# Performance work log

Measured on AMD Instinct MI355X. Metric: run time of the kernel, lower is better.

## Reference

```python
import jax, jax.numpy as jnp
import numpy as np

SEQ_LEN = 4096
EMBED_DIM = 1280
NUM_HEADS = 16
HEAD_DIM = EMBED_DIM // NUM_HEADS  # 80
SCALING = float(np.sqrt(HEAD_DIM))  # NOTE: source multiplies by sqrt(head_dim)
NEG_INF = float(np.finfo(np.float32).min)


def rotate_half(x):
    x1, x2 = jnp.split(x, 2, axis=-1)
    return jnp.concatenate((-x2, x1), axis=-1)


def setup_inputs() -> dict:
    key = jax.random.key(0)
    ks = jax.random.split(key, 7)
    s = 0.02
    hidden_states = jax.random.normal(ks[0], (SEQ_LEN, EMBED_DIM), dtype=jnp.float32)
    w_qkv = jax.random.normal(ks[1], (3 * EMBED_DIM, EMBED_DIM), dtype=jnp.float32) * s
    b_qkv = jax.random.normal(ks[2], (3 * EMBED_DIM,), dtype=jnp.float32) * s
    w_proj = jax.random.normal(ks[3], (EMBED_DIM, EMBED_DIM), dtype=jnp.float32) * s
    b_proj = jax.random.normal(ks[4], (EMBED_DIM,), dtype=jnp.float32) * s
    # rotary angles: theta duplicated to head_dim (emb = cat(rope, rope))
    inv_freq = 1.0 / (10000.0 ** (jnp.arange(0, HEAD_DIM // 2, dtype=jnp.float32) * 2.0 / HEAD_DIM))
    pos = jnp.arange(SEQ_LEN, dtype=jnp.float32)
    freqs = pos[:, None] * inv_freq[None, :]            # [S, hd/2]
    emb = jnp.concatenate((freqs, freqs), axis=-1)       # [S, hd]
    cos = jnp.cos(emb)
    sin = jnp.sin(emb)
    # 4 packed images of 1024 patches each
    cu_seqlens = jnp.array([0, 1024, 2048, 3072, 4096], dtype=jnp.int32)
    return {
        "hidden_states": hidden_states,
        "w_qkv": w_qkv, "b_qkv": b_qkv,
        "w_proj": w_proj, "b_proj": b_proj,
        "cos": cos, "sin": sin,
        "cu_seqlens": cu_seqlens,
    }


def reference(hidden_states, w_qkv, b_qkv, w_proj, b_proj, cos, sin, cu_seqlens):
    S = hidden_states.shape[0]
    # packed QKV projection
    qkv = hidden_states @ w_qkv.T + b_qkv                  # [S, 3D]
    qkv = qkv.reshape(S, 3, NUM_HEADS, HEAD_DIM)
    q, k, v = qkv[:, 0], qkv[:, 1], qkv[:, 2]              # [S, H, hd]
    # fp32 RoPE (broadcast cos/sin over heads)
    c = cos[:, None, :].astype(jnp.float32)
    sn = sin[:, None, :].astype(jnp.float32)
    qf, kf = q.astype(jnp.float32), k.astype(jnp.float32)
    q = (qf * c + rotate_half(qf) * sn).astype(q.dtype)
    k = (kf * c + rotate_half(kf) * sn).astype(k.dtype)
    # block-diagonal mask from cu_seqlens: same segment -> 0, else -inf
    pos = jnp.arange(S)
    seg = jnp.searchsorted(cu_seqlens, pos, side="right") - 1  # [S]
    bias = jnp.where(seg[:, None] == seg[None, :], 0.0, NEG_INF)  # [S, S]
    # dense attention over whole packed sequence (as in source)
    scores = jnp.einsum("shd,thd->hst", q, k) * SCALING + bias[None]
    weights = jax.nn.softmax(scores.astype(jnp.float32), axis=-1).astype(q.dtype)
    attn = jnp.einsum("hst,thd->shd", weights, v).reshape(S, EMBED_DIM)
    return attn @ w_proj.T + b_proj
```

## Files before the change

### kernel.cpp

```cpp
#include <hip/hip_runtime.h>

#define SEQ   4096
#define EMB   1280
#define NH    16
#define HD    80
#define HDP   96
#define O3    3840
#define SEGLEN 1024
#define NSEG  4
#define QSCALE (8.94427190999915878564f * 1.44269504088896340736f)

typedef unsigned short u16;
typedef __attribute__((ext_vector_type(8))) _Float16 f16x8;
typedef __attribute__((ext_vector_type(4))) _Float16 f16x4;
typedef __attribute__((ext_vector_type(2))) __fp16   h16x2;
typedef __attribute__((ext_vector_type(4))) float    f32x4;

__device__ __forceinline__ float ex2(float x) { return __builtin_amdgcn_exp2f(x); }

__device__ __forceinline__ u16 f2h(float f) {
  union { _Float16 h; u16 u; } v; v.h = (_Float16)f; return v.u;
}
__device__ __forceinline__ float h2f(u16 b) {
  union { u16 u; _Float16 h; } v; v.u = b; return (float)v.h;
}
__device__ __forceinline__ f32x4 exp2_4(f32x4 x) {
  f32x4 r; r.x = ex2(x.x); r.y = ex2(x.y); r.z = ex2(x.z); r.w = ex2(x.w); return r;
}
__device__ __forceinline__ f16x4 pk4(f32x4 s) {
  union { h16x2 h[2]; f16x4 f; } u;
  u.h[0] = __builtin_amdgcn_cvt_pkrtz(s.x, s.y);
  u.h[1] = __builtin_amdgcn_cvt_pkrtz(s.z, s.w);
  return u.f;
}
__device__ __forceinline__ void gl2lds16(const u16* g, u16* l) {
  __builtin_amdgcn_global_load_lds(
      (const __attribute__((address_space(1))) unsigned int*)g,
      (__attribute__((address_space(3))) unsigned int*)l, 16, 0, 0);
}

#define CVT_N1 (SEQ * EMB / 4)
#define CVT_N2 (O3 * EMB / 4)
#define CVT_N3 (EMB * EMB / 4)
__global__ void cvt_all_kernel(const float* __restrict__ a, const float* __restrict__ b,
                               const float* __restrict__ c, u16* __restrict__ oa,
                               u16* __restrict__ ob, u16* __restrict__ oc) {
  int i = blockIdx.x * blockDim.x + threadIdx.x;
  const float* src; u16* dst; int j = i;
  if (j < CVT_N1)                { src = a; dst = oa; }
  else if (j < CVT_N1 + CVT_N2)  { src = b; dst = ob; j -= CVT_N1; }
  else                           { src = c; dst = oc; j -= CVT_N1 + CVT_N2; }
  float4 f = ((const float4*)src)[j];
  union { u16 h[4]; uint2 v; } o;
  o.h[0] = f2h(f.x); o.h[1] = f2h(f.y); o.h[2] = f2h(f.z); o.h[3] = f2h(f.w);
  ((uint2*)dst)[j] = o.v;
}

template<int OUTF>
__global__ __launch_bounds__(256)
void gemm_bias_kernel(const u16* __restrict__ A, const u16* __restrict__ W,
                      const float* __restrict__ bias, void* __restrict__ Cout,
                      int N, int K) {
  __shared__ u16 As[128][64];
  __shared__ u16 Bs[128][64];
  const int tid  = threadIdx.x;
  const int bm   = blockIdx.y, bn = blockIdx.x;
  const int lane = tid & 63;
  const int wid  = tid >> 6;
  const int wm   = (wid >> 1) * 64, wn = (wid & 1) * 64;
  const int lr   = lane & 15, quad = lane >> 4;

  f32x4 acc[4][4];
  const f32x4 z4 = {0.f, 0.f, 0.f, 0.f};
  #pragma unroll
  for (int i = 0; i < 4; ++i)
    #pragma unroll
    for (int j = 0; j < 4; ++j) acc[i][j] = z4;

  const int arow = tid >> 3;
  const int acol = (((tid & 7) ^ (arow & 7)) * 8);
  const u16* Ab = A + (size_t)(bm * 128) * K;
  const u16* Wb = W + (size_t)(bn * 128) * K;
  u16* AsL = &As[0][0] + tid * 8;
  u16* BsL = &Bs[0][0] + tid * 8;

  for (int kt = 0; kt < K; kt += 64) {
    #pragma unroll
    for (int r = 0; r < 4; ++r) {
      gl2lds16(&Ab[(size_t)(arow + r * 32) * K + kt + acol], AsL + r * 2048);
      gl2lds16(&Wb[(size_t)(arow + r * 32) * K + kt + acol], BsL + r * 2048);
    }
    __syncthreads();
    #pragma unroll
    for (int k32 = 0; k32 < 2; ++k32) {
      const int c = (((k32 * 4 + quad) ^ (lr & 7)) * 8);
      f16x8 aF[4], bF[4];
      #pragma unroll
      for (int i = 0; i < 4; ++i) {
        aF[i] = *(const f16x8*)&As[wm + i * 16 + lr][c];
        bF[i] = *(const f16x8*)&Bs[wn + i * 16 + lr][c];
      }
      #pragma unroll
      for (int i = 0; i < 4; ++i)
        #pragma unroll
        for (int j = 0; j < 4; ++j)
          acc[i][j] = __builtin_amdgcn_mfma_f32_16x16x32_f16(aF[i], bF[j], acc[i][j], 0, 0, 0);
    }
    __syncthreads();
  }

  #pragma unroll
  for (int i = 0; i < 4; ++i) {
    int rowb = bm * 128 + wm + i * 16 + quad * 4;
    #pragma unroll
    for (int j = 0; j < 4; ++j) {
      int col = bn * 128 + wn + j * 16 + lr;
      float bv = bias[col];
      #pragma unroll
      for (int r = 0; r < 4; ++r) {
        float v = acc[i][j][r] + bv;
        if (OUTF) ((float*)Cout)[(size_t)(rowb + r) * N + col] = v;
        else      ((u16*)Cout)[(size_t)(rowb + r) * N + col] = f2h(v);
      }
    }
  }
}

__global__ __launch_bounds__(512, 2)
void gemm256_kernel(const u16* __restrict__ A, const u16* __restrict__ W,
                    const float* __restrict__ bias, u16* __restrict__ Cout,
                    int N, int K) {
  __shared__ u16 As[2][256][64];
  __shared__ u16 Bs[2][256][64];
  const int tid  = threadIdx.x;
  const int bm   = blockIdx.y, bn = blockIdx.x;
  const int lane = tid & 63;
  const int wid  = tid >> 6;
  const int wm   = wid >> 2;
  const int wn   = wid & 3;
  const int lr   = lane & 15, quad = lane >> 4;
  const int NT   = K >> 6;

  const u16* Ab = A + (size_t)(bm * 256) * K;
  const u16* Wb = W + (size_t)(bn * 256) * K;

  const int srr  = tid >> 3;
  const int scol = ((tid & 7) ^ (srr & 7)) << 3;
  const u16* ApL = Ab + (size_t)srr * K + scol;
  const u16* WpL = Wb + (size_t)srr * K + scol;

  auto stA = [&](int b, int row0, int t) {
    gl2lds16(ApL + (size_t)row0 * K + t * 64,        &As[b][row0][0]      + tid * 8);
    gl2lds16(ApL + (size_t)(row0 + 64) * K + t * 64, &As[b][row0 + 64][0] + tid * 8);
  };
  auto stB = [&](int b, int row0, int t) {
    gl2lds16(WpL + (size_t)row0 * K + t * 64,        &Bs[b][row0][0]      + tid * 8);
    gl2lds16(WpL + (size_t)(row0 + 64) * K + t * 64, &Bs[b][row0 + 64][0] + tid * 8);
  };

  f32x4 acc[8][4];
  const f32x4 z4 = {0.f, 0.f, 0.f, 0.f};
  #pragma unroll
  for (int i = 0; i < 8; ++i)
    #pragma unroll
    for (int j = 0; j < 4; ++j) acc[i][j] = z4;

  stA(0, 0, 0); stA(0, 128, 0);
  stB(0, 0, 0); stB(0, 128, 0);
  stA(1, 0, 1);
  asm volatile("s_waitcnt vmcnt(2)" ::: "memory");
  __builtin_amdgcn_s_barrier();

  for (int t = 0; t < NT; ++t) {
    const int buf = t & 1, nb = buf ^ 1;
    #pragma unroll
    for (int mq = 0; mq < 2; ++mq) {
      #pragma unroll
      for (int k32 = 0; k32 < 2; ++k32) {
        const int c = (((k32 * 4 + quad) ^ (lr & 7)) << 3);
        f16x8 aF[4], bF[4];
        #pragma unroll
        for (int i = 0; i < 4; ++i)
          aF[i] = *(const f16x8*)&As[buf][mq * 128 + wm * 64 + i * 16 + lr][c];
        #pragma unroll
        for (int j = 0; j < 4; ++j)
          bF[j] = *(const f16x8*)&Bs[buf][wn * 64 + j * 16 + lr][c];
        __builtin_amdgcn_sched_barrier(0);
        if (mq == 0 && k32 == 0) {
          if (t + 1 < NT) { stB(nb, 0, t + 1); stA(nb, 128, t + 1); }
        } else if (mq == 0 && k32 == 1) {
          if (t + 1 < NT) stB(nb, 128, t + 1);
        } else if (mq == 1 && k32 == 0) {
          if (t + 2 < NT) stA(buf, 0, t + 2);
        }
        __builtin_amdgcn_s_barrier();
        asm volatile("s_waitcnt lgkmcnt(0)" ::: "memory");
        __builtin_amdgcn_sched_barrier(0);
        __builtin_amdgcn_s_setprio(1);
        #pragma unroll
        for (int i = 0; i < 4; ++i)
          #pragma unroll
          for (int j = 0; j < 4; ++j)
            acc[mq * 4 + i][j] =
                __builtin_amdgcn_mfma_f32_16x16x32_f16(aF[i], bF[j], acc[mq * 4 + i][j], 0, 0, 0);
        __builtin_amdgcn_s_setprio(0);
        if (mq == 1 && k32 == 1) {
          if (t < NT - 2) asm volatile("s_waitcnt vmcnt(2)" ::: "memory");
          else            asm volatile("s_waitcnt vmcnt(0)" ::: "memory");
        }
        __builtin_amdgcn_s_barrier();
        __builtin_amdgcn_sched_barrier(0);
      }
    }
  }

  #pragma unroll
  for (int mq = 0; mq < 2; ++mq) {
    #pragma unroll
    for (int i = 0; i < 4; ++i) {
      const int rowb = bm * 256 + mq * 128 + wm * 64 + i * 16 + quad * 4;
      #pragma unroll
      for (int j = 0; j < 4; ++j) {
        const int col = bn * 256 + wn * 64 + j * 16 + lr;
        const float bv = bias[col];
        #pragma unroll
        for (int r = 0; r < 4; ++r)
          Cout[(size_t)(rowb + r) * N + col] = f2h(acc[mq * 4 + i][j][r] + bv);
      }
    }
  }
}

__global__ __launch_bounds__(256)
void rope_reorg_kernel(const u16* __restrict__ qkv, const float* __restrict__ cosp,
                       const float* __restrict__ sinp, u16* __restrict__ Qp,
                       u16* __restrict__ Kp, u16* __restrict__ Vt) {
  __shared__ u16 Qs[64][80];
  __shared__ u16 Ks[64][80];
  __shared__ u16 Vs[64][88];
  const int tid = threadIdx.x;
  const int s0 = blockIdx.x * 64;
  const int h  = blockIdx.y;

  for (int t = tid; t < 640; t += 256) {
    int r = t / 10, c = (t % 10) * 8;
    size_t g = (size_t)(s0 + r) * O3 + h * HD + c;
    *(uint4*)&Qs[r][c] = *(const uint4*)&qkv[g];
    *(uint4*)&Ks[r][c] = *(const uint4*)&qkv[g + EMB];
    *(uint4*)&Vs[r][c] = *(const uint4*)&qkv[g + 2 * EMB];
  }
  __syncthreads();

  for (int t = tid; t < 64 * 24; t += 256) {
    int r = t / 24, d4 = (t % 24) * 4;
    int s = s0 + r;
    size_t po = ((size_t)h * SEQ + s) * HDP + d4;
    if (d4 >= HD) {
      uint2 z = make_uint2(0, 0);
      *(uint2*)&Qp[po] = z; *(uint2*)&Kp[po] = z;
      continue;
    }
    float4 cv = *(const float4*)&cosp[(size_t)s * HD + d4];
    float4 sv = *(const float4*)&sinp[(size_t)s * HD + d4];
    int dp4 = (d4 < 40) ? d4 + 40 : d4 - 40;
    float sgn = (d4 < 40) ? -1.f : 1.f;
    union { u16 h[4]; uint2 v; } oq, ok;
    const float* cp = (const float*)&cv;
    const float* sp = (const float*)&sv;
    #pragma unroll
    for (int j = 0; j < 4; ++j) {
      float q  = h2f(Qs[r][d4 + j]),  k  = h2f(Ks[r][d4 + j]);
      float qp = h2f(Qs[r][dp4 + j]), kp = h2f(Ks[r][dp4 + j]);
      oq.h[j] = f2h((q * cp[j] + sgn * qp * sp[j]) * QSCALE);
      ok.h[j] = f2h(k * cp[j] + sgn * kp * sp[j]);
    }
    *(uint2*)&Qp[po] = oq.v;
    *(uint2*)&Kp[po] = ok.v;
  }

  for (int t = tid; t < HD * 8; t += 256) {
    int d = t / 8, sc = (t % 8) * 8;
    union { u16 h[8]; uint4 v; } o;
    #pragma unroll
    for (int j = 0; j < 8; ++j) o.h[j] = Vs[sc + j][d];
    *(uint4*)&Vt[((size_t)(h * HD + d)) * SEQ + s0 + sc] = o.v;
  }
}

__global__ __launch_bounds__(256)
void attn_kernel(const u16* __restrict__ Qp, const u16* __restrict__ Kp,
                 const u16* __restrict__ Vt, u16* __restrict__ attnO) {
  __shared__ u16 K_l[64][96];
  __shared__ u16 V_l[96][64];

  const int tid = threadIdx.x;
  const int lane = tid & 63, w = tid >> 6;
  const int lr = lane & 15, quad = lane >> 4;
  const int h = blockIdx.y, sg = blockIdx.z;
  const int seg0 = sg * SEGLEN;
  const int q0b = seg0 + blockIdx.x * 64;

  f16x8 qF[3];
  {
    int qrow = q0b + w * 16 + lr;
    #pragma unroll
    for (int kc = 0; kc < 3; ++kc)
      qF[kc] = *(const f16x8*)&Qp[((size_t)h * SEQ + qrow) * HDP + kc * 32 + quad * 8];
  }

  {
    u16 val = (tid < 16) ? (u16)0x3C00 : (u16)0;
    u16* q = &V_l[80][0] + tid * 4;
    q[0] = val; q[1] = val; q[2] = val; q[3] = val;
  }

  const u16* Kbase = Kp + ((size_t)h * SEQ + seg0) * HDP;
  const u16* Vbase = Vt + (size_t)h * HD * SEQ + seg0;
  const u16* pK[3]; u16* dK[3];
  const u16* pV[3]; u16* dV[3];
  #pragma unroll
  for (int t = 0; t < 3; ++t) {
    int s = t * 256 + tid;
    int r = s / 12, c = s % 12;
    int ck = (c & ~3) | ((c & 3) ^ ((r >> 1) & 3));
    pK[t] = Kbase + (size_t)r * HDP + ck * 8;
    dK[t] = &K_l[0][0] + s * 8;
    int rv = s / 8, cv = s % 8;
    int cg = cv ^ (rv & 7);
    pV[t] = Vbase + (size_t)rv * SEQ + cg * 8;
    dV[t] = &V_l[0][0] + s * 8;
  }

  const f32x4 z4 = {0.f, 0.f, 0.f, 0.f};
  float m_r = -3.0e38f;
  f32x4 Oacc[6];
  #pragma unroll
  for (int n = 0; n < 6; ++n) Oacc[n] = z4;

  const int kswz = (lr >> 1) & 3;

  for (int kt = 0; kt < SEGLEN; kt += 64) {
    gl2lds16(pK[0], dK[0]); gl2lds16(pK[1], dK[1]); gl2lds16(pK[2], dK[2]);
    gl2lds16(pV[0], dV[0]); gl2lds16(pV[1], dV[1]);
    if (tid < 128) gl2lds16(pV[2], dV[2]);
    #pragma unroll
    for (int t = 0; t < 3; ++t) { pK[t] += 64 * HDP; pV[t] += 64; }
    __syncthreads();

    f32x4 S[4];
    __builtin_amdgcn_s_setprio(1);
    #pragma unroll
    for (int ct = 0; ct < 4; ++ct) {
      S[ct] = z4;
      #pragma unroll
      for (int kc = 0; kc < 3; ++kc) {
        f16x8 kF = *(const f16x8*)&K_l[ct * 16 + lr][kc * 32 + ((quad ^ kswz) << 3)];
        S[ct] = __builtin_amdgcn_mfma_f32_16x16x32_f16(kF, qF[kc], S[ct], 0, 0, 0);
      }
    }
    __builtin_amdgcn_s_setprio(0);

    float mx = fmaxf(fmaxf(S[0].x, S[0].y), fmaxf(S[0].z, S[0].w));
    #pragma unroll
    for (int ct = 1; ct < 4; ++ct)
      mx = fmaxf(mx, fmaxf(fmaxf(S[ct].x, S[ct].y), fmaxf(S[ct].z, S[ct].w)));
    mx = fmaxf(mx, __shfl_xor(mx, 16, 64));
    mx = fmaxf(mx, __shfl_xor(mx, 32, 64));
    float mnew = fmaxf(m_r, mx);
    float alpha = ex2(m_r - mnew);
    m_r = mnew;

    f32x4 mv = {mnew, mnew, mnew, mnew};
    #pragma unroll
    for (int ct = 0; ct < 4; ++ct) S[ct] = exp2_4(S[ct] - mv);

    if (__ballot(alpha != 1.0f)) {
      f32x4 al;
      al.x = __shfl(alpha, quad * 4 + 0, 64);
      al.y = __shfl(alpha, quad * 4 + 1, 64);
      al.z = __shfl(alpha, quad * 4 + 2, 64);
      al.w = __shfl(alpha, quad * 4 + 3, 64);
      #pragma unroll
      for (int n = 0; n < 6; ++n) Oacc[n] *= al;
    }

    f16x4 pF[4];
    #pragma unroll
    for (int ct = 0; ct < 4; ++ct) pF[ct] = pk4(S[ct]);

    __builtin_amdgcn_s_setprio(1);
    #pragma unroll
    for (int ct = 0; ct < 4; ++ct) {
      const int cchunk = 2 * ct + (quad >> 1);
      #pragma unroll
      for (int n = 0; n < 6; ++n) {
        int vrow = n * 16 + lr;
        const u16* vp = &V_l[0][0] + vrow * 64 + ((cchunk ^ (vrow & 7)) << 3) + ((quad & 1) << 2);
        f16x4 vF = *(const f16x4*)vp;
        Oacc[n] = __builtin_amdgcn_mfma_f32_16x16x16f16(pF[ct], vF, Oacc[n], 0, 0, 0);
      }
    }
    __builtin_amdgcn_s_setprio(0);
    __syncthreads();
  }

  f32x4 linv;
  linv.x = 1.0f / __shfl(Oacc[5].x, quad << 4, 64);
  linv.y = 1.0f / __shfl(Oacc[5].y, quad << 4, 64);
  linv.z = 1.0f / __shfl(Oacc[5].z, quad << 4, 64);
  linv.w = 1.0f / __shfl(Oacc[5].w, quad << 4, 64);
  #pragma unroll
  for (int n = 0; n < 5; ++n) {
    int rowb = q0b + w * 16 + quad * 4;
    int col = h * HD + n * 16 + lr;
    attnO[(size_t)(rowb + 0) * EMB + col] = f2h(Oacc[n].x * linv.x);
    attnO[(size_t)(rowb + 1) * EMB + col] = f2h(Oacc[n].y * linv.y);
    attnO[(size_t)(rowb + 2) * EMB + col] = f2h(Oacc[n].z * linv.z);
    attnO[(size_t)(rowb + 3) * EMB + col] = f2h(Oacc[n].w * linv.w);
  }
}

extern "C" void kernel_launch(void* const* d_in, const int* in_sizes, int n_in,
                              void* d_out, int out_size, void* d_ws, size_t ws_size,
                              hipStream_t stream) {
  const float* hs     = (const float*)d_in[0];
  const float* w_qkv  = (const float*)d_in[1];
  const float* b_qkv  = (const float*)d_in[2];
  const float* w_proj = (const float*)d_in[3];
  const float* b_proj = (const float*)d_in[4];
  const float* cosp   = (const float*)d_in[5];
  const float* sinp   = (const float*)d_in[6];
  float* out = (float*)d_out;

  char* p = (char*)d_ws;
  auto take = [&](size_t bytes) { char* q = p; p += (bytes + 255) & ~(size_t)255; return q; };
  u16* hsH    = (u16*)take((size_t)SEQ * EMB * 2);
  u16* wqkvH  = (u16*)take((size_t)O3 * EMB * 2);
  u16* wprojH = (u16*)take((size_t)EMB * EMB * 2);
  u16* qkvO   = (u16*)take((size_t)SEQ * O3 * 2);
  u16* Qp     = (u16*)take((size_t)NH * SEQ * HDP * 2);
  u16* Kp     = (u16*)take((size_t)NH * SEQ * HDP * 2);
  u16* Vt     = (u16*)take((size_t)NH * HD * SEQ * 2);
  u16* attnH  = (u16*)take((size_t)SEQ * EMB * 2);

  int ncvt = (CVT_N1 + CVT_N2 + CVT_N3) / 256;
  cvt_all_kernel<<<ncvt, 256, 0, stream>>>(hs, w_qkv, w_proj, hsH, wqkvH, wprojH);

  gemm256_kernel<<<dim3(O3 / 256, SEQ / 256), 512, 0, stream>>>(hsH, wqkvH, b_qkv, qkvO, O3, EMB);

  rope_reorg_kernel<<<dim3(SEQ / 64, NH), 256, 0, stream>>>(qkvO, cosp, sinp, Qp, Kp, Vt);

  attn_kernel<<<dim3(SEGLEN / 64, NH, NSEG), 256, 0, stream>>>(Qp, Kp, Vt, attnH);

  gemm_bias_kernel<1><<<dim3(EMB / 128, SEQ / 128), 256, 0, stream>>>(attnH, wprojH, b_proj, out, EMB, EMB);
}
```

Measured before the change: 238.4 us.

## Triple-buffer K/V tiles with async prefetch and 128-row attention blocks

The attention kernel now uses three LDS buffers for K and V tiles and issues global-to-LDS loads two tiles ahead, using vmcnt waits plus a single barrier per iteration instead of load-then-sync. Block size doubles to 512 threads (128 query rows) so each K/V tile is shared by eight waves, halving K/V global traffic per query. The aim is to hide load latency behind MFMA work. The cost is more LDS per block (about 72KB), which lowers occupancy, and the hand-written waitcnt counts are fragile.

```diff
diff --git a/kernel.cpp b/kernel.cpp
--- a/kernel.cpp
+++ b/kernel.cpp
@@ -287,18 +287,19 @@
   }
 }
 
-__global__ __launch_bounds__(256)
+__global__ __launch_bounds__(512)
 void attn_kernel(const u16* __restrict__ Qp, const u16* __restrict__ Kp,
                  const u16* __restrict__ Vt, u16* __restrict__ attnO) {
-  __shared__ u16 K_l[64][96];
-  __shared__ u16 V_l[96][64];
+  __shared__ u16 K_l[3][64][96];
+  __shared__ u16 V_l[3][96][64];
+  const int BUFSZ = 6144;
 
   const int tid = threadIdx.x;
   const int lane = tid & 63, w = tid >> 6;
   const int lr = lane & 15, quad = lane >> 4;
   const int h = blockIdx.y, sg = blockIdx.z;
   const int seg0 = sg * SEGLEN;
-  const int q0b = seg0 + blockIdx.x * 64;
+  const int q0b = seg0 + blockIdx.x * 128;
 
   f16x8 qF[3];
   {
@@ -307,29 +308,47 @@
     for (int kc = 0; kc < 3; ++kc)
       qF[kc] = *(const f16x8*)&Qp[((size_t)h * SEQ + qrow) * HDP + kc * 32 + quad * 8];
   }
+  asm volatile("" :: "v"(qF[0]), "v"(qF[1]), "v"(qF[2]));
+  asm volatile("s_waitcnt vmcnt(0)" ::: "memory");
 
   {
-    u16 val = (tid < 16) ? (u16)0x3C00 : (u16)0;
-    u16* q = &V_l[80][0] + tid * 4;
-    q[0] = val; q[1] = val; q[2] = val; q[3] = val;
+    u16 val = (tid < 32) ? (u16)0x3C00 : (u16)0;
+    #pragma unroll
+    for (int b = 0; b < 3; ++b) {
+      u16* q = &V_l[0][0][0] + b * BUFSZ + 80 * 64 + tid * 2;
+      q[0] = val; q[1] = val;
+    }
   }
 
   const u16* Kbase = Kp + ((size_t)h * SEQ + seg0) * HDP;
   const u16* Vbase = Vt + (size_t)h * HD * SEQ + seg0;
-  const u16* pK[3]; u16* dK[3];
-  const u16* pV[3]; u16* dV[3];
+  const u16* pG[3]; u16* dB[3]; int gAdv[3];
   #pragma unroll
   for (int t = 0; t < 3; ++t) {
-    int s = t * 256 + tid;
-    int r = s / 12, c = s % 12;
-    int ck = (c & ~3) | ((c & 3) ^ ((r >> 1) & 3));
-    pK[t] = Kbase + (size_t)r * HDP + ck * 8;
-    dK[t] = &K_l[0][0] + s * 8;
-    int rv = s / 8, cv = s % 8;
-    int cg = cv ^ (rv & 7);
-    pV[t] = Vbase + (size_t)rv * SEQ + cg * 8;
-    dV[t] = &V_l[0][0] + s * 8;
-  }
+    int s = t * 512 + tid;
+    if (s < 768) {
+      int r = s / 12, c = s % 12;
+      int ck = (c & ~3) | ((c & 3) ^ ((r >> 1) & 3));
+      pG[t] = Kbase + (size_t)r * HDP + ck * 8;
+      dB[t] = &K_l[0][0][0] + s * 8;
+      gAdv[t] = 64 * HDP;
+    } else {
+      int sv = (s < 1408) ? s - 768 : s - 1408;
+      int rv = sv / 8, cv = sv % 8;
+      int cg = cv ^ (rv & 7);
+      pG[t] = Vbase + (size_t)rv * SEQ + cg * 8;
+      dB[t] = &V_l[0][0][0] + sv * 8;
+      gAdv[t] = 64;
+    }
+  }
+
+  auto stage_adv = [&](int b) {
+    #pragma unroll
+    for (int t = 0; t < 3; ++t) {
+      gl2lds16(pG[t], dB[t] + b * BUFSZ);
+      pG[t] += gAdv[t];
+    }
+  };
 
   const f32x4 z4 = {0.f, 0.f, 0.f, 0.f};
   float m_r = -3.0e38f;
@@ -339,13 +358,18 @@
 
   const int kswz = (lr >> 1) & 3;
 
+  stage_adv(0);
+  stage_adv(1);
+  asm volatile("s_waitcnt vmcnt(3) lgkmcnt(0)" ::: "memory");
+  __builtin_amdgcn_s_barrier();
+  __builtin_amdgcn_sched_barrier(0);
+
+  int buf = 0, sb = 2;
   for (int kt = 0; kt < SEGLEN; kt += 64) {
-    gl2lds16(pK[0], dK[0]); gl2lds16(pK[1], dK[1]); gl2lds16(pK[2], dK[2]);
-    gl2lds16(pV[0], dV[0]); gl2lds16(pV[1], dV[1]);
-    if (tid < 128) gl2lds16(pV[2], dV[2]);
-    #pragma unroll
-    for (int t = 0; t < 3; ++t) { pK[t] += 64 * HDP; pV[t] += 64; }
-    __syncthreads();
+    if (kt + 128 < SEGLEN) stage_adv(sb);
+
+    const u16* kb = &K_l[0][0][0] + buf * BUFSZ;
+    const u16* vb = &V_l[0][0][0] + buf * BUFSZ;
 
     f32x4 S[4];
     __builtin_amdgcn_s_setprio(1);
@@ -354,7 +378,7 @@
       S[ct] = z4;
       #pragma unroll
       for (int kc = 0; kc < 3; ++kc) {
-        f16x8 kF = *(const f16x8*)&K_l[ct * 16 + lr][kc * 32 + ((quad ^ kswz) << 3)];
+        f16x8 kF = *(const f16x8*)&kb[(ct * 16 + lr) * 96 + kc * 32 + ((quad ^ kswz) << 3)];
         S[ct] = __builtin_amdgcn_mfma_f32_16x16x32_f16(kF, qF[kc], S[ct], 0, 0, 0);
       }
     }
@@ -395,13 +419,20 @@
       #pragma unroll
       for (int n = 0; n < 6; ++n) {
         int vrow = n * 16 + lr;
-        const u16* vp = &V_l[0][0] + vrow * 64 + ((cchunk ^ (vrow & 7)) << 3) + ((quad & 1) << 2);
+        const u16* vp = vb + vrow * 64 + ((cchunk ^ (vrow & 7)) << 3) + ((quad & 1) << 2);
         f16x4 vF = *(const f16x4*)vp;
         Oacc[n] = __builtin_amdgcn_mfma_f32_16x16x16f16(pF[ct], vF, Oacc[n], 0, 0, 0);
       }
     }
     __builtin_amdgcn_s_setprio(0);
-    __syncthreads();
+
+    if (kt + 128 < SEGLEN) asm volatile("s_waitcnt vmcnt(3)" ::: "memory");
+    else                   asm volatile("s_waitcnt vmcnt(0)" ::: "memory");
+    __builtin_amdgcn_s_barrier();
+    __builtin_amdgcn_sched_barrier(0);
+
+    buf = (buf == 2) ? 0 : buf + 1;
+    sb  = (sb == 2) ? 0 : sb + 1;
   }
 
   f32x4 linv;
@@ -450,7 +481,7 @@
 
   rope_reorg_kernel<<<dim3(SEQ / 64, NH), 256, 0, stream>>>(qkvO, cosp, sinp, Qp, Kp, Vt);
 
-  attn_kernel<<<dim3(SEGLEN / 64, NH, NSEG), 256, 0, stream>>>(Qp, Kp, Vt, attnH);
+  attn_kernel<<<dim3(SEGLEN / 128, NH, NSEG), 512, 0, stream>>>(Qp, Kp, Vt, attnH);
 
   gemm_bias_kernel<1><<<dim3(EMB / 128, SEQ / 128), 256, 0, stream>>>(attnH, wprojH, b_proj, out, EMB, EMB);
 }
```

New measurement: 241.9 us. No clear change (+1.5%).
